# Kernel optimization log

Hardware: AMD Instinct MI355X
Metric: run time of the kernel (lower is better)

## Reference

```python
import math
import jax, jax.numpy as jnp
import numpy as np

IN_CH = 512
OUT_CH = 512
KSIZE = 3
STYLE_DIM = 512
EPS = 1e-8


def setup_inputs() -> dict:
    key = jax.random.key(0)
    ks = jax.random.split(key, 8)
    B, H, W = 16, 32, 32
    x = jax.random.normal(ks[0], (B, IN_CH, H, W), dtype=jnp.float32)
    style = jax.random.normal(ks[1], (B, STYLE_DIM), dtype=jnp.float32)
    noise = jax.random.normal(ks[2], (B, 1, 2 * H, 2 * W), dtype=jnp.float32)
    # learned params (matching torch init semantics)
    conv_weight = jax.random.normal(ks[3], (OUT_CH, IN_CH, KSIZE, KSIZE), dtype=jnp.float32)
    mod_weight = jax.random.normal(ks[4], (IN_CH, STYLE_DIM), dtype=jnp.float32)
    mod_bias = jnp.ones((IN_CH,), dtype=jnp.float32)  # bias_init=1
    noise_weight = jax.random.normal(ks[5], (1,), dtype=jnp.float32) * 0.1
    act_bias = jnp.zeros((OUT_CH,), dtype=jnp.float32)
    return {"x": x, "style": style, "noise": noise, "conv_weight": conv_weight,
            "mod_weight": mod_weight, "mod_bias": mod_bias,
            "noise_weight": noise_weight, "act_bias": act_bias}


def _blur_kernel_2d():
    k = jnp.array([1.0, 3.0, 3.0, 1.0], dtype=jnp.float32)
    k2 = k[None, :] * k[:, None]
    k2 = k2 / k2.sum()
    return k2 * 4.0  # upsample_factor**2


def _styled_conv_up(x, style, conv_weight, mod_weight, mod_bias,
                    noise_weight, act_bias, noise):
    B, C_in, H, W = x.shape
    # EqualLinear modulation: scale = 1/sqrt(style_dim), lr_mul=1
    s = style @ (mod_weight * (1.0 / math.sqrt(STYLE_DIM))).T + mod_bias  # [B, C_in]
    # modulate + demodulate per-sample weights
    wscale = 1.0 / math.sqrt(C_in * KSIZE * KSIZE)
    w = wscale * conv_weight[None] * s[:, None, :, None, None]  # [B, out, in, k, k]
    demod = jax.lax.rsqrt(jnp.sum(w * w, axis=(2, 3, 4)) + EPS)  # [B, out]
    w = w * demod[:, :, None, None, None]
    # conv_transpose2d(stride=2, padding=0) == lhs_dilated conv with spatially
    # flipped kernel. torch passes weight as (in, out, k, k); equivalent OIHW
    # forward kernel is flip(w) with layout (out, in, k, k).
    w_flip = jnp.flip(w, axis=(-2, -1))

    def single(xi, wi):  # xi [in,H,W], wi [out,in,k,k]
        return jax.lax.conv_general_dilated(
            xi[None], wi, window_strides=(1, 1),
            padding=[(KSIZE - 1, KSIZE - 1)] * 2,
            lhs_dilation=(2, 2),
            dimension_numbers=("NCHW", "OIHW", "NCHW"))[0]

    out = jax.vmap(single)(x, w_flip)  # [B, out, 2H+1, 2W+1] for k=3
    # Blur: upfirdn2d(kernel=4x4, pad=(1,1)) -> depthwise valid conv
    Bc, Co, Ho, Wo = out.shape
    kb = _blur_kernel_2d()[None, None]  # [1,1,4,4] (symmetric, flip is a no-op)
    out = jax.lax.conv_general_dilated(
        out.reshape(Bc * Co, 1, Ho, Wo), kb, window_strides=(1, 1),
        padding=[(1, 1), (1, 1)],
        dimension_numbers=("NCHW", "OIHW", "NCHW"))
    out = out.reshape(Bc, Co, Ho + 2 - 3, Wo + 2 - 3)  # [B, out, 2H, 2W]
    # noise injection + FusedLeakyReLU (slope 0.2, scale sqrt(2))
    out = out + noise_weight * noise
    out = jax.nn.leaky_relu(out + act_bias.reshape(1, -1, 1, 1), 0.2) * math.sqrt(2.0)
    return out


def reference(x, style, noise, conv_weight, mod_weight, mod_bias,
              noise_weight, act_bias):
    return _styled_conv_up(x, style, conv_weight, mod_weight, mod_bias,
                           noise_weight, act_bias, noise)
```

## Files before the change

### kernel.cpp

```cpp
#include <hip/hip_runtime.h>
#include <math.h>


typedef __attribute__((ext_vector_type(8))) __bf16 bf16x8;
typedef __attribute__((ext_vector_type(4))) float f32x4;

#define WSCALE 0.014731391274719739f
#define SSCALE 0.044194173824159216f

__device__ __forceinline__ unsigned short f2bf(float f) {
  unsigned u = __builtin_bit_cast(unsigned, f);
  u += 0x7fff + ((u >> 16) & 1);
  return (unsigned short)(u >> 16);
}
__device__ __forceinline__ float bf2f(unsigned short h) {
  unsigned u = ((unsigned)h) << 16;
  return __builtin_bit_cast(float, u);
}

__global__ __launch_bounds__(256) void k_style(
    const float* __restrict__ style, const float* __restrict__ mod_w,
    const float* __restrict__ mod_b, float* __restrict__ s_out) {
  int wid  = (blockIdx.x * 256 + threadIdx.x) >> 6;
  int lane = threadIdx.x & 63;
  int b = wid >> 9, ic = wid & 511;
  float acc = 0.f;
  for (int j = lane; j < 512; j += 64)
    acc += style[b * 512 + j] * mod_w[ic * 512 + j];
  for (int off = 32; off > 0; off >>= 1) acc += __shfl_down(acc, off);
  if (lane == 0) s_out[b * 512 + ic] = acc * SSCALE + mod_b[ic];
}

__device__ const int SLABTAP[9] = {0, 2, 6, 8, 1, 7, 3, 5, 4};
__device__ const int SLABOFF[4] = {0, 4, 6, 8};
__device__ const int TAPN[4]    = {4, 2, 2, 1};
__device__ const int TOFFp[4][4] = {{0,-1,-34,-35},{0,-34,0,0},{0,-1,0,0},{0,0,0,0}};

__global__ __launch_bounds__(256) void k_w2(
    const float* __restrict__ conv_w, unsigned short* __restrict__ W2,
    float* __restrict__ w2s) {
  __shared__ float t[4608];
  const int oc = blockIdx.x;
  for (int i = threadIdx.x; i < 4608; i += 256) t[i] = conv_w[oc * 4608 + i];
  __syncthreads();
  for (int i = threadIdx.x; i < 4608; i += 256) {
    int tg = i >> 9, ic = i & 511;
    W2[((size_t)(tg * 512 + oc)) * 512 + ic] = f2bf(t[ic * 9 + SLABTAP[tg]]);
  }
  for (int i = threadIdx.x; i < 512; i += 256) {
    float a = 0.f;
    #pragma unroll
    for (int tg = 0; tg < 9; tg++) { float w = t[i * 9 + tg]; a += w * w; }
    w2s[oc * 512 + i] = a;
  }
}

__global__ __launch_bounds__(256) void k_demod(
    const float* __restrict__ w2s, const float* __restrict__ s,
    float* __restrict__ dscale) {
  int wid  = (blockIdx.x * 256 + threadIdx.x) >> 6;
  int lane = threadIdx.x & 63;
  int b = wid >> 9, oc = wid & 511;
  float acc = 0.f;
  for (int ic = lane; ic < 512; ic += 64) {
    float sv = s[b * 512 + ic];
    acc += sv * sv * w2s[oc * 512 + ic];
  }
  for (int off = 32; off > 0; off >>= 1) acc += __shfl_down(acc, off);
  if (lane == 0)
    dscale[b * 512 + oc] = WSCALE * rsqrtf(WSCALE * WSCALE * acc + 1e-8f);
}

__global__ __launch_bounds__(256) void k_xs2(
    const float* __restrict__ x, const float* __restrict__ s,
    unsigned short* __restrict__ S2) {
  __shared__ float xt[64][65];
  const int b = blockIdx.z, ic0 = blockIdx.y * 64, r0 = blockIdx.x * 2;
  for (int i = threadIdx.x; i < 4096; i += 256) {
    int icL = i >> 6, pxL = i & 63;
    int gr = r0 + (pxL >> 5), gc = pxL & 31;
    xt[icL][pxL] = x[((b * 512 + ic0 + icL) * 32 + gr) * 32 + gc] * s[b * 512 + ic0 + icL];
  }
  __syncthreads();
  for (int i = threadIdx.x; i < 512; i += 256) {
    int pxL = i >> 3, icO = i & 7;
    unsigned short tmp[8];
    #pragma unroll
    for (int k = 0; k < 8; k++) tmp[k] = f2bf(xt[icO * 8 + k][pxL]);
    int gr = r0 + (pxL >> 5), gc = pxL & 31;
    int R = (gr + 1) * 34 + (gc + 1);
    *(uint4*)(&S2[((size_t)b * 1156 + R) * 512 + ic0 + icO * 8]) = *(const uint4*)tmp;
  }
}

__global__ void k_zero(unsigned short* __restrict__ S2) {
  int b = blockIdx.y, id = blockIdx.x;
  int ry, rx;
  if (id < 34)       { ry = 0;        rx = id; }
  else if (id < 68)  { ry = 33;       rx = id - 34; }
  else if (id < 100) { ry = id - 67;  rx = 0; }
  else               { ry = id - 99;  rx = 33; }
  ((unsigned*)(S2 + ((size_t)b * 1156 + ry * 34 + rx) * 512))[threadIdx.x] = 0;
}

__global__ __launch_bounds__(256, 2) void k_gemm(
    const unsigned short* __restrict__ S2, const unsigned short* __restrict__ W2,
    const float* __restrict__ dscale, unsigned short* __restrict__ I,
    int b_base, int nTot) {
  __shared__ __align__(16) unsigned short As[128][64];
  __shared__ __align__(16) unsigned short Bs[256][64];

  const int mt = blockIdx.x;
  const int nt = blockIdx.y;
  const int p  = blockIdx.z;
  const int m0 = mt * 128, n0 = nt * 256;
  const int tid = threadIdx.x, lane = tid & 63;
  const int wv = tid >> 6, wm = wv >> 1, wn = wv & 1;
  const int l15 = lane & 15, quad = lane >> 4;
  const int ntap = TAPN[p], soff = SLABOFF[p];
  const int kq = tid & 7;

  int gRow[8];
  #pragma unroll
  for (int it = 0; it < 8; it++) {
    int r = it * 32 + (tid >> 3);
    int n = n0 + r;
    if (n < nTot) {
      int bl = n / 1089;
      int u = n - bl * 1089;
      int uy = u / 33, ux = u - uy * 33;
      gRow[it] = (b_base + bl) * 1156 + (uy + 1) * 34 + (ux + 1);
    } else gRow[it] = -1;
  }

  f32x4 acc[4][8];
  #pragma unroll
  for (int m = 0; m < 4; m++)
    #pragma unroll
    for (int n = 0; n < 8; n++) acc[m][n] = (f32x4)0.f;

  const int kend = ntap * 512;
  #pragma unroll 1
  for (int k0 = 0; k0 < kend; k0 += 64) {
    const int tj   = k0 >> 9;
    const int icw  = k0 & 511;
    const int off  = TOFFp[p][tj];
    const int slab = soff + tj;
    __syncthreads();
    #pragma unroll
    for (int it = 0; it < 4; it++) {
      int r = it * 32 + (tid >> 3);
      uint4 v = *(const uint4*)(W2 + ((size_t)(slab * 512 + m0 + r)) * 512 + icw + kq * 8);
      *(uint4*)(&As[r][(kq ^ (r & 7)) * 8]) = v;
    }
    #pragma unroll
    for (int it = 0; it < 8; it++) {
      int r = it * 32 + (tid >> 3);
      uint4 v = make_uint4(0u, 0u, 0u, 0u);
      if (gRow[it] >= 0)
        v = *(const uint4*)(S2 + (size_t)(gRow[it] + off) * 512 + icw + kq * 8);
      *(uint4*)(&Bs[r][(kq ^ (r & 7)) * 8]) = v;
    }
    __syncthreads();
    #pragma unroll
    for (int kk = 0; kk < 2; kk++) {
      bf16x8 af[4], bfr[8];
      #pragma unroll
      for (int m = 0; m < 4; m++) {
        int r = wm * 64 + m * 16 + l15;
        af[m] = *(const bf16x8*)(&As[r][((kk * 4 + quad) ^ (r & 7)) * 8]);
      }
      #pragma unroll
      for (int n = 0; n < 8; n++) {
        int r = wn * 128 + n * 16 + l15;
        bfr[n] = *(const bf16x8*)(&Bs[r][((kk * 4 + quad) ^ (r & 7)) * 8]);
      }
      #pragma unroll
      for (int m = 0; m < 4; m++)
        #pragma unroll
        for (int n = 0; n < 8; n++)
          acc[m][n] = __builtin_amdgcn_mfma_f32_16x16x32_bf16(af[m], bfr[n], acc[m][n], 0, 0, 0);
    }
  }

  #pragma unroll
  for (int n = 0; n < 8; n++) {
    int nf = n0 + wn * 128 + n * 16 + l15;
    if (nf < nTot) {
      int bl = nf / 1089;
      int ul = nf - bl * 1089;
      const size_t Ibase = ((size_t)(bl * 4 + p) * 512) * 1096;
      #pragma unroll
      for (int m = 0; m < 4; m++) {
        int oc = m0 + wm * 64 + m * 16 + quad * 4;
        #pragma unroll
        for (int r = 0; r < 4; r++) {
          float ds = dscale[(b_base + bl) * 512 + oc + r];
          I[Ibase + (size_t)(oc + r) * 1096 + ul] = f2bf(acc[m][n][r] * ds);
        }
      }
    }
  }
}

__global__ __launch_bounds__(256) void k_blur(
    const unsigned short* __restrict__ I, const float* __restrict__ noise,
    const float* __restrict__ noise_w, const float* __restrict__ act_b,
    float* __restrict__ out, int b_base) {
  __shared__ __align__(16) unsigned short Ism[4][1096];
  __shared__ float V[64][67];
  const int oc = blockIdx.x, bl = blockIdx.y, b = b_base + bl;
  for (int i = threadIdx.x; i < 548; i += 256) {
    int p = i / 137, w = i - p * 137;
    *(uint4*)(&Ism[p][w * 8]) =
        *(const uint4*)(I + ((size_t)(bl * 4 + p) * 512 + oc) * 1096 + w * 8);
  }
  __syncthreads();
  for (int i = threadIdx.x; i < 2112; i += 256) {
    int r = i / 66, col = i - r * 66;
    int px_ = (col >= 33), ux = col - 33 * px_;
    float v0 = (r >= 1) ? bf2f(Ism[2 + px_][(r - 1) * 33 + ux]) : 0.f;
    float a_ = bf2f(Ism[px_][r * 33 + ux]);
    float b_ = bf2f(Ism[2 + px_][r * 33 + ux]);
    float c_ = bf2f(Ism[px_][(r + 1) * 33 + ux]);
    float d_ = bf2f(Ism[2 + px_][(r + 1) * 33 + ux]);
    V[2 * r][col]     = 0.25f * v0 + 0.75f * a_ + 0.75f * b_ + 0.25f * c_;
    V[2 * r + 1][col] = 0.25f * a_ + 0.75f * b_ + 0.75f * c_ + 0.25f * d_;
  }
  __syncthreads();
  const float nw = noise_w[0], ab = act_b[oc];
  for (int i = threadIdx.x; i < 2048; i += 256) {
    int qy = i >> 5, rx = i & 31;
    float w0 = (rx >= 1) ? V[qy][33 + rx - 1] : 0.f;
    float a_ = V[qy][rx];
    float b_ = V[qy][33 + rx];
    float c_ = V[qy][rx + 1];
    float d_ = V[qy][33 + rx + 1];
    float o0 = 0.25f * w0 + 0.75f * a_ + 0.75f * b_ + 0.25f * c_;
    float o1 = 0.25f * a_ + 0.75f * b_ + 0.75f * c_ + 0.25f * d_;
    const float2 nv = *(const float2*)(noise + b * 4096 + qy * 64 + 2 * rx);
    o0 += nw * nv.x + ab;  o1 += nw * nv.y + ab;
    o0 = (o0 > 0.f ? o0 : 0.2f * o0) * 1.4142135623730951f;
    o1 = (o1 > 0.f ? o1 : 0.2f * o1) * 1.4142135623730951f;
    float2 ov = make_float2(o0, o1);
    *(float2*)(out + (((size_t)b * 512 + oc) * 64 + qy) * 64 + 2 * rx) = ov;
  }
}

extern "C" void kernel_launch(void* const* d_in, const int* in_sizes, int n_in,
                              void* d_out, int out_size, void* d_ws, size_t ws_size,
                              hipStream_t stream) {
  const float* x       = (const float*)d_in[0];
  const float* style   = (const float*)d_in[1];
  const float* noise   = (const float*)d_in[2];
  const float* conv_w  = (const float*)d_in[3];
  const float* mod_w   = (const float*)d_in[4];
  const float* mod_b   = (const float*)d_in[5];
  const float* noise_w = (const float*)d_in[6];
  const float* act_b   = (const float*)d_in[7];
  float* out = (float*)d_out;

  char* ws = (char*)d_ws;
  float*          s_ws = (float*)ws;
  float*          d_sc = (float*)(ws + 32768);
  float*          w2s  = (float*)(ws + 65536);
  unsigned short* S2   = (unsigned short*)(ws + 65536 + 1048576);
  unsigned short* W2   = (unsigned short*)(ws + 65536 + 1048576 + 18939904);
  unsigned short* I    = (unsigned short*)(ws + 65536 + 1048576 + 18939904 + 4718592);
  const size_t fixed = 65536ull + 1048576ull + 18939904ull + 4718592ull;
  const size_t per_b = (size_t)4 * 512 * 1096 * 2;

  int nb = 16;
  if (ws_size < fixed + 16 * per_b) nb = 8;
  if (ws_size < fixed + 8 * per_b)  nb = 4;
  if (ws_size < fixed + 4 * per_b)  nb = 2;
  if (ws_size < fixed + 2 * per_b)  nb = 1;

  k_style<<<2048, 256, 0, stream>>>(style, mod_w, mod_b, s_ws);
  k_w2<<<512, 256, 0, stream>>>(conv_w, W2, w2s);
  k_demod<<<2048, 256, 0, stream>>>(w2s, s_ws, d_sc);
  k_xs2<<<dim3(16, 8, 16), 256, 0, stream>>>(x, s_ws, S2);
  k_zero<<<dim3(132, 16), 256, 0, stream>>>(S2);
  for (int b0 = 0; b0 < 16; b0 += nb) {
    int nTot = nb * 1089;
    k_gemm<<<dim3(4, (nTot + 255) / 256, 4), 256, 0, stream>>>(S2, W2, d_sc, I, b0, nTot);
    k_blur<<<dim3(512, nb), 256, 0, stream>>>(I, noise, noise_w, act_b, out, b0);
  }
}
```

Before: 483.5 us.

## Tile GEMM per batch with XCD-aware block swizzle and hoisted demod scales

The GEMM grid is now one dimension and decoded per batch, phase, N-tile and M-tile. Block IDs are permuted so that consecutive logical tiles, which share activations and weights, land on the same XCD and can reuse its L2. Tiles no longer span batch boundaries, which removes per-row divisions, and the demodulation scales are loaded once per thread before the store loop. The cost is extra padded work: each batch's 1089 rows are rounded up to five 256-row tiles, so more MFMA work is wasted on masked rows than before.

```diff
diff --git a/kernel.cpp b/kernel.cpp
--- a/kernel.cpp
+++ b/kernel.cpp
@@ -105,15 +105,18 @@
 
 __global__ __launch_bounds__(256, 2) void k_gemm(
     const unsigned short* __restrict__ S2, const unsigned short* __restrict__ W2,
-    const float* __restrict__ dscale, unsigned short* __restrict__ I,
-    int b_base, int nTot) {
+    const float* __restrict__ dscale, unsigned short* __restrict__ I, int b_base) {
   __shared__ __align__(16) unsigned short As[128][64];
   __shared__ __align__(16) unsigned short Bs[256][64];
 
-  const int mt = blockIdx.x;
-  const int nt = blockIdx.y;
-  const int p  = blockIdx.z;
+  const int nblk = gridDim.x, qq = nblk >> 3, lid = blockIdx.x;
+  const int swz = (lid & 7) * qq + (lid >> 3);
+  const int bl = swz / 80;  int rr = swz - bl * 80;
+  const int p  = rr / 20;   rr -= p * 20;
+  const int nt = rr >> 2, mt = rr & 3;
+  const int b  = b_base + bl;
   const int m0 = mt * 128, n0 = nt * 256;
+
   const int tid = threadIdx.x, lane = tid & 63;
   const int wv = tid >> 6, wm = wv >> 1, wn = wv & 1;
   const int l15 = lane & 15, quad = lane >> 4;
@@ -125,11 +128,9 @@
   for (int it = 0; it < 8; it++) {
     int r = it * 32 + (tid >> 3);
     int n = n0 + r;
-    if (n < nTot) {
-      int bl = n / 1089;
-      int u = n - bl * 1089;
-      int uy = u / 33, ux = u - uy * 33;
-      gRow[it] = (b_base + bl) * 1156 + (uy + 1) * 34 + (ux + 1);
+    if (n < 1089) {
+      int uy = n / 33, ux = n - uy * 33;
+      gRow[it] = b * 1156 + (uy + 1) * 34 + (ux + 1);
     } else gRow[it] = -1;
   }
 
@@ -183,21 +184,23 @@
     }
   }
 
+  float dsv[4][4];
+  #pragma unroll
+  for (int m = 0; m < 4; m++)
+    #pragma unroll
+    for (int r = 0; r < 4; r++)
+      dsv[m][r] = dscale[b * 512 + m0 + wm * 64 + m * 16 + quad * 4 + r];
+  const size_t Ibase = ((size_t)(bl * 4 + p) * 512) * 1096;
   #pragma unroll
   for (int n = 0; n < 8; n++) {
     int nf = n0 + wn * 128 + n * 16 + l15;
-    if (nf < nTot) {
-      int bl = nf / 1089;
-      int ul = nf - bl * 1089;
-      const size_t Ibase = ((size_t)(bl * 4 + p) * 512) * 1096;
+    if (nf < 1089) {
       #pragma unroll
       for (int m = 0; m < 4; m++) {
         int oc = m0 + wm * 64 + m * 16 + quad * 4;
         #pragma unroll
-        for (int r = 0; r < 4; r++) {
-          float ds = dscale[(b_base + bl) * 512 + oc + r];
-          I[Ibase + (size_t)(oc + r) * 1096 + ul] = f2bf(acc[m][n][r] * ds);
-        }
+        for (int r = 0; r < 4; r++)
+          I[Ibase + (size_t)(oc + r) * 1096 + nf] = f2bf(acc[m][n][r] * dsv[m][r]);
       }
     }
   }
@@ -282,8 +285,7 @@
   k_xs2<<<dim3(16, 8, 16), 256, 0, stream>>>(x, s_ws, S2);
   k_zero<<<dim3(132, 16), 256, 0, stream>>>(S2);
   for (int b0 = 0; b0 < 16; b0 += nb) {
-    int nTot = nb * 1089;
-    k_gemm<<<dim3(4, (nTot + 255) / 256, 4), 256, 0, stream>>>(S2, W2, d_sc, I, b0, nTot);
+    k_gemm<<<nb * 80, 256, 0, stream>>>(S2, W2, d_sc, I, b0);
     k_blur<<<dim3(512, nb), 256, 0, stream>>>(I, noise, noise_w, act_b, out, b0);
   }
 }
```

Measured after the change: 439.3 us. 1.1x faster.
